# Performance work log

Hardware: AMD Instinct MI355X
Metric: run time of the kernel (lower is better)

Reference implementation:

```python
import jax, jax.numpy as jnp
import numpy as np

B, U, L, H, M = 4, 16, 128, 768, 256   # docs, utterances/doc, tokens/utt, hidden, mentions/doc
HID = 150                               # Score MLP hidden dim
N_CLUSTERS = 32


def setup_inputs() -> dict:
    key = jax.random.key(0)
    ks = jax.random.split(key, 8)
    hidden = jax.random.normal(ks[0], (B, U, L, H), jnp.float32)

    rng = np.random.default_rng(0)
    span_utt = rng.integers(0, U, (B, M))
    span_start = rng.integers(0, L - 8, (B, M))
    span_end = span_start + rng.integers(1, 9, (B, M))  # span length in [1, 8]

    # coreference labels: label[i, j] = 1 iff j is a true antecedent (j < i, same cluster);
    # if mention i has no antecedent, label[i, i] = 1 (the epsilon / new-entity slot).
    clusters = rng.integers(0, N_CLUSTERS, (B, M))
    same = clusters[:, :, None] == clusters[:, None, :]
    ant = same & np.tril(np.ones((M, M), bool), -1)
    labels = ant.astype(np.float32)
    diag = np.arange(M)
    labels[:, diag, diag] = (~ant.any(-1)).astype(np.float32)

    scale = 0.02
    W1 = jax.random.normal(ks[1], (3 * H, HID), jnp.float32) * scale
    W2 = jax.random.normal(ks[2], (HID, HID), jnp.float32) * scale
    W3 = jax.random.normal(ks[3], (HID, 1), jnp.float32) * scale
    return {
        "hidden": hidden,
        "span_utt": jnp.asarray(span_utt, jnp.int32),
        "span_start": jnp.asarray(span_start, jnp.int32),
        "span_end": jnp.asarray(span_end, jnp.int32),
        "labels": jnp.asarray(labels),
        "W1": W1, "b1": jnp.zeros((HID,), jnp.float32),
        "W2": W2, "b2": jnp.zeros((HID,), jnp.float32),
        "W3": W3, "b3": jnp.zeros((1,), jnp.float32),
    }


def reference(hidden, span_utt, span_start, span_end, labels, W1, b1, W2, b2, W3, b3):
    # ---- span mean-pooling (EntityEncoder, aggr='mean') ----
    pos = jnp.arange(L)
    mask = (pos[None, None, :] >= span_start[..., None]) & (pos[None, None, :] < span_end[..., None])
    w = mask.astype(hidden.dtype) / (span_end - span_start)[..., None].astype(hidden.dtype)  # [B,M,L]
    gathered = jnp.take_along_axis(hidden, span_utt[:, :, None, None], axis=1)  # [B,M,L,H]
    pooled = jnp.einsum('bml,bmlh->bmh', w, gathered)  # [B,M,H]

    # ---- pairwise antecedent scoring (PairScorer / Score MLP, dropout=eval) ----
    ii, jj = np.tril_indices(M, -1)  # static pair indices, P = M(M-1)/2
    # concat(i_g, j_g, i_g*j_g) @ W1  ==  i_g@W1a + j_g@W1b + (i_g*j_g)@W1c
    W1a, W1b, W1c = W1[:H], W1[H:2 * H], W1[2 * H:]
    hi = pooled @ W1a   # [B,M,HID]
    hj = pooled @ W1b   # [B,M,HID]
    prod = pooled[:, ii] * pooled[:, jj]                    # [B,P,H]
    h1 = jax.nn.relu(hi[:, ii] + hj[:, jj] + prod @ W1c + b1)
    h2 = jax.nn.relu(h1 @ W2 + b2)
    s = (h2 @ W3 + b3)[..., 0]  # [B,P]

    # ---- per-mention ragged softmax, padded to [M, M] with -1000 ----
    # row i has logits s_ij for j<i plus epsilon=0 at j=i (diagonal of zeros matrix)
    logits = jnp.zeros((B, M, M), hidden.dtype).at[:, ii, jj].set(s)
    valid = jnp.tril(jnp.ones((M, M), bool))
    probs = jax.nn.softmax(jnp.where(valid, logits, -1e30), axis=-1)
    probs = jnp.where(valid, probs, jnp.asarray(-1000.0, hidden.dtype))

    # ---- compute_loss ----
    eps = 1e-8
    prob_sum = jnp.sum(jnp.clip(probs * labels, eps, 1.0 - eps), axis=-1)  # [B,M]
    loss = -jnp.sum(jnp.log(prob_sum))
    return loss
```

## Files before the change

kernel.cpp:

```cpp
#include <hip/hip_runtime.h>
#include <hip/hip_bf16.h>

#define B_ 4
#define U_ 16
#define L_ 128
#define H_ 768
#define M_ 256
#define HID_ 150

typedef _Float16 half8 __attribute__((ext_vector_type(8)));
typedef _Float16 half4t __attribute__((ext_vector_type(4)));
typedef float floatx4 __attribute__((ext_vector_type(4)));
typedef float floatx16 __attribute__((ext_vector_type(16)));

__device__ __forceinline__ void gl_lds16(const _Float16* g, _Float16* l)
{
    __builtin_amdgcn_global_load_lds(
        (const __attribute__((address_space(1))) unsigned int*)g,
        (__attribute__((address_space(3))) unsigned int*)l, 16, 0, 0);
}

__global__ __launch_bounds__(256) void prep_pool_kernel(
    const float* __restrict__ W1, const float* __restrict__ W2,
    const float* __restrict__ b2, const float* __restrict__ W3,
    const float* __restrict__ hidden, const int* __restrict__ sutt,
    const int* __restrict__ sstart, const int* __restrict__ send,
    _Float16* __restrict__ W1cs, _Float16* __restrict__ W2s,
    _Float16* __restrict__ W1abs, float2* __restrict__ bw,
    _Float16* __restrict__ pooledh)
{
    if (blockIdx.x >= 1540) {
        const int bm = (blockIdx.x - 1540) * 4 + (threadIdx.x >> 6);
        const int lane = threadIdx.x & 63;
        const int b  = bm >> 8;
        const int u  = sutt[bm];
        const int st = sstart[bm];
        const int en = send[bm];
        const float inv = 1.0f / (float)(en - st);
        const float* src = hidden + ((size_t)(b * U_ + u) * L_) * H_ + lane * 12;
        float4 s[3];
        #pragma unroll
        for (int q = 0; q < 3; ++q) s[q] = make_float4(0.f, 0.f, 0.f, 0.f);
        for (int l = st; l < en; ++l) {
            const float* p = src + (size_t)l * H_;
            #pragma unroll
            for (int q = 0; q < 3; ++q) {
                float4 v = *(const float4*)(p + q * 4);
                s[q].x += v.x; s[q].y += v.y; s[q].z += v.z; s[q].w += v.w;
            }
        }
        _Float16* gp = pooledh + (size_t)bm * H_ + lane * 12;
        #pragma unroll
        for (int q = 0; q < 3; ++q) {
            half4t hv;
            hv[0] = (_Float16)(s[q].x * inv); hv[1] = (_Float16)(s[q].y * inv);
            hv[2] = (_Float16)(s[q].z * inv); hv[3] = (_Float16)(s[q].w * inv);
            *(half4t*)(gp + q * 4) = hv;
        }
        return;
    }
    int idx = blockIdx.x * 256 + threadIdx.x;
    if (blockIdx.x == 0 && threadIdx.x < 160) {
        int n = threadIdx.x;
        bw[n] = (n < HID_) ? make_float2(b2[n], W3[n]) : make_float2(0.f, 0.f);
    }
    if (idx < 122880) {
        int k = idx / 160, n = idx - k * 160;
        float v = (n < HID_) ? W1[(size_t)(2 * H_ + k) * HID_ + n] : 0.f;
        W1cs[(k >> 4) * 2560 + (n >> 5) * 512 +
             (((n & 31) | (((k >> 3) & 1) << 5)) << 3) + (k & 7)] = (_Float16)v;
        return;
    }
    idx -= 122880;
    if (idx < 25600) {
        int k = idx / 160, n = idx - k * 160;
        float v = (k < HID_ && n < HID_) ? W2[(size_t)k * HID_ + n] : 0.f;
        W2s[(k >> 4) * 2560 + (n >> 5) * 512 +
            (((n & 31) | (((k >> 3) & 1) << 5)) << 3) + (k & 7)] = (_Float16)v;
        return;
    }
    idx -= 25600;
    if (idx < 245760) {
        int k = idx / 320, n = idx - k * 320;
        float v = 0.f;
        if (n < HID_) v = W1[(size_t)k * HID_ + n];
        else if (n >= 160 && n < 160 + HID_) v = W1[(size_t)(H_ + k) * HID_ + (n - 160)];
        W1abs[(k >> 5) * 10240 + (n >> 4) * 512 +
              (((n & 15) | (((k >> 3) & 3) << 4)) << 3) + (k & 7)] = (_Float16)v;
    }
}

__global__ __launch_bounds__(256) void hihj_kernel(
    const _Float16* __restrict__ pooledh, const float* __restrict__ b1,
    const _Float16* __restrict__ W1abs,
    float* __restrict__ hiF, float* __restrict__ hjT)
{
    __shared__ __align__(16) _Float16 spool[16 * 776];
    const int blk = blockIdx.x;
    const int tid = threadIdx.x;
    for (int e = tid; e < 16 * 96; e += 256) {
        int r = e / 96, c = e - r * 96;
        *(half8*)&spool[r * 776 + c * 8] =
            *(const half8*)&pooledh[(size_t)(blk * 16 + r) * H_ + c * 8];
    }
    __syncthreads();

    const int w = tid >> 6, lane = tid & 63;
    const int g = lane >> 4, l15 = lane & 15;
    floatx4 acc[5];
    #pragma unroll
    for (int u5 = 0; u5 < 5; ++u5) acc[u5] = (floatx4){0.f, 0.f, 0.f, 0.f};
    const _Float16* aB = &spool[l15 * 776 + g * 8];
    for (int kc = 0; kc < 24; ++kc) {
        half8 av = *(const half8*)(aB + kc * 32);
        #pragma unroll
        for (int u5 = 0; u5 < 5; ++u5) {
            const int u = w * 5 + u5;
            half8 bv = *(const half8*)(W1abs + (size_t)((kc * 20 + u) * 64 + lane) * 8);
            acc[u5] = __builtin_amdgcn_mfma_f32_16x16x32_f16(av, bv, acc[u5], 0, 0, 0);
        }
    }
    const int row0 = blk * 16 + g * 4;
    #pragma unroll
    for (int u5 = 0; u5 < 5; ++u5) {
        const int n = (w * 5 + u5) * 16 + l15;
        if (n < HID_) {
            float b1v = b1[n];
            #pragma unroll
            for (int r = 0; r < 4; ++r)
                hiF[(size_t)(row0 + r) * 160 + n] = acc[u5][r] + b1v;
        } else if (n >= 160 && n < 160 + HID_) {
            *(float4*)&hjT[(size_t)(n - 160) * 1024 + row0] =
                make_float4(acc[u5][0], acc[u5][1], acc[u5][2], acc[u5][3]);
        }
    }
}

__global__ __launch_bounds__(128, 2) void pair_mlp_kernel(
    const _Float16* __restrict__ pooledh,
    const float* __restrict__ hiF, const float* __restrict__ hjT,
    const _Float16* __restrict__ W1cs, const _Float16* __restrict__ W2s,
    const float2* __restrict__ bw, const float* __restrict__ b3,
    float* __restrict__ logits)
{
    __shared__ __align__(16) _Float16 smem[3 * 5120];

    int q = blockIdx.x;
    const int b = q / 576;
    int r = q - b * 576;
    int jt = 0;
    while (r >= 128 - 16 * jt) { r -= 128 - 16 * jt; ++jt; }
    const int p = 16 * jt + r;
    const int i0 = 2 * p, j0 = jt * 32;
    const int bm = b * M_;
    const int w = threadIdx.x >> 6;
    const int lane = threadIdx.x & 63;
    const int c31 = lane & 31;
    const int hw = lane >> 5;

    _Float16* h1w = smem + w * 5440;

    const _Float16* pjp = pooledh + (size_t)(bm + j0 + c31) * H_ + (hw << 3);
    const _Float16* pip = pooledh + (size_t)(bm + i0 + w) * H_ + (hw << 3);

    floatx16 acc1[5];
    #pragma unroll
    for (int t1 = 0; t1 < 5; ++t1)
        #pragma unroll
        for (int e = 0; e < 16; ++e) acc1[t1][e] = 0.f;

    {
        const _Float16* gW = W1cs + (size_t)(5 * w) * 512 + lane * 8;
        #pragma unroll
        for (int c = 0; c < 5; ++c)
            gl_lds16(gW + c * 512, smem + (5 * w + c) * 512);
        #pragma unroll
        for (int c = 0; c < 5; ++c)
            gl_lds16(gW + 5120 + c * 512, smem + 5120 + (5 * w + c) * 512);
    }
    half8 Apj0[2], Apj1[2], Ai0[2], Ai1[2];
    Apj0[0] = *(const half8*)(pjp);
    Apj1[0] = *(const half8*)(pjp + 16);
    Ai0[0]  = *(const half8*)(pip);
    Ai1[0]  = *(const half8*)(pip + 16);
    asm volatile("s_waitcnt vmcnt(11)" ::: "memory");
    __builtin_amdgcn_s_barrier();
    __builtin_amdgcn_sched_barrier(0);

    #pragma unroll
    for (int kc = 0; kc < 24; ++kc) {
        const int cur = kc & 1, nxt = (kc + 1) & 1;
        const _Float16* Wcur = smem + (kc % 3) * 5120;
        if (kc < 23) {
            const int kb = (kc + 1) * 32;
            Apj0[nxt] = *(const half8*)(pjp + kb);
            Apj1[nxt] = *(const half8*)(pjp + kb + 16);
            Ai0[nxt]  = *(const half8*)(pip + kb);
            Ai1[nxt]  = *(const half8*)(pip + kb + 16);
        }
        if (kc < 22) {
            const _Float16* gW = W1cs + (size_t)(kc + 2) * 5120
                                 + (5 * w) * 512 + lane * 8;
            _Float16* Wd = smem + ((kc + 2) % 3) * 5120;
            #pragma unroll
            for (int c = 0; c < 5; ++c)
                gl_lds16(gW + c * 512, Wd + (5 * w + c) * 512);
        }
        {
            half8 a = Ai0[cur] * Apj0[cur];
            #pragma unroll
            for (int t1 = 0; t1 < 5; ++t1) {
                half8 wf = *(const half8*)&Wcur[t1 * 512 + lane * 8];
                acc1[t1] = __builtin_amdgcn_mfma_f32_32x32x16_f16(wf, a, acc1[t1], 0, 0, 0);
            }
        }
        {
            half8 a = Ai1[cur] * Apj1[cur];
            #pragma unroll
            for (int t1 = 0; t1 < 5; ++t1) {
                half8 wf = *(const half8*)&Wcur[(5 + t1) * 512 + lane * 8];
                acc1[t1] = __builtin_amdgcn_mfma_f32_32x32x16_f16(wf, a, acc1[t1], 0, 0, 0);
            }
        }
        if (kc < 22)       asm volatile("s_waitcnt vmcnt(11)" ::: "memory");
        else if (kc == 22) asm volatile("s_waitcnt vmcnt(6)" ::: "memory");
        if (kc < 23) {
            __builtin_amdgcn_s_barrier();
            __builtin_amdgcn_sched_barrier(0);
        }
    }
    __syncthreads();

    const int jcol = bm + j0 + c31;
    #pragma unroll
    for (int t1 = 0; t1 < 5; ++t1) {
        #pragma unroll
        for (int qd = 0; qd < 4; ++qd) {
            const int n1 = t1 * 32 + 8 * qd + 4 * hw;
            float hj0 = hjT[(size_t)(n1 + 0) * 1024 + jcol];
            float hj1 = hjT[(size_t)(n1 + 1) * 1024 + jcol];
            float hj2 = hjT[(size_t)(n1 + 2) * 1024 + jcol];
            float hj3 = hjT[(size_t)(n1 + 3) * 1024 + jcol];
            float4 hiv = *(const float4*)&hiF[(size_t)(bm + i0 + w) * 160 + n1];
            half4t hv;
            hv[0] = (_Float16)fmaxf(acc1[t1][4 * qd + 0] + hiv.x + hj0, 0.f);
            hv[1] = (_Float16)fmaxf(acc1[t1][4 * qd + 1] + hiv.y + hj1, 0.f);
            hv[2] = (_Float16)fmaxf(acc1[t1][4 * qd + 2] + hiv.z + hj2, 0.f);
            hv[3] = (_Float16)fmaxf(acc1[t1][4 * qd + 3] + hiv.w + hj3, 0.f);
            *(half4t*)&h1w[c31 * 170 + n1] = hv;
        }
    }
    __syncthreads();

    const float b3v = b3[0];
    floatx16 acc2[5];
    #pragma unroll
    for (int t2 = 0; t2 < 5; ++t2)
        #pragma unroll
        for (int e = 0; e < 16; ++e) acc2[t2][e] = 0.f;

    half8 W2b[2][5], h1b[2];
    #pragma unroll
    for (int c = 0; c < 2; ++c) {
        const _Float16* wb = W2s + (size_t)(c * 5) * 512 + lane * 8;
        #pragma unroll
        for (int t2 = 0; t2 < 5; ++t2) W2b[c][t2] = *(const half8*)(wb + t2 * 512);
        h1b[c] = *(const half8*)&h1w[c31 * 170 + c * 16 + hw * 8];
    }
    for (int kc2 = 0; kc2 < 10; ++kc2) {
        const int cur = kc2 & 1;
        half8 nw[5], nh;
        if (kc2 < 8) {
            const _Float16* wb = W2s + (size_t)((kc2 + 2) * 5) * 512 + lane * 8;
            #pragma unroll
            for (int t2 = 0; t2 < 5; ++t2) nw[t2] = *(const half8*)(wb + t2 * 512);
            nh = *(const half8*)&h1w[c31 * 170 + (kc2 + 2) * 16 + hw * 8];
        }
        #pragma unroll
        for (int t2 = 0; t2 < 5; ++t2)
            acc2[t2] = __builtin_amdgcn_mfma_f32_32x32x16_f16(
                W2b[cur][t2], h1b[cur], acc2[t2], 0, 0, 0);
        if (kc2 < 8) {
            #pragma unroll
            for (int t2 = 0; t2 < 5; ++t2) W2b[cur][t2] = nw[t2];
            h1b[cur] = nh;
        }
    }

    float sown = 0.f;
    #pragma unroll
    for (int t2 = 0; t2 < 5; ++t2) {
        #pragma unroll
        for (int qd = 0; qd < 4; ++qd) {
            const int n2 = t2 * 32 + 8 * qd + 4 * hw;
            float4 bw01 = *(const float4*)&bw[n2];
            float4 bw23 = *(const float4*)&bw[n2 + 2];
            sown += fmaxf(acc2[t2][4 * qd + 0] + bw01.x, 0.f) * bw01.y;
            sown += fmaxf(acc2[t2][4 * qd + 1] + bw01.z, 0.f) * bw01.w;
            sown += fmaxf(acc2[t2][4 * qd + 2] + bw23.x, 0.f) * bw23.y;
            sown += fmaxf(acc2[t2][4 * qd + 3] + bw23.z, 0.f) * bw23.w;
        }
    }
    float s = sown + __shfl_xor(sown, 32);
    const int i = i0 + w;
    const int j = j0 + c31;
    if (lane < 32 && j < i)
        logits[(size_t)(bm + i) * M_ + j] = s + b3v;
}

__global__ __launch_bounds__(256) void loss_kernel(
    const float* __restrict__ logits, const float* __restrict__ labels,
    float* __restrict__ out)
{
    const int bm = blockIdx.x;
    const int i  = bm & (M_ - 1);
    const int j  = threadIdx.x;
    __shared__ float red[4];
    __shared__ float bcast;

    float val = (j < i) ? logits[(size_t)bm * M_ + j]
                        : ((j == i) ? 0.0f : -1e30f);

    float m = val;
    #pragma unroll
    for (int off = 32; off >= 1; off >>= 1) m = fmaxf(m, __shfl_down(m, off, 64));
    const int wave = j >> 6, lane = j & 63;
    if (lane == 0) red[wave] = m;
    __syncthreads();
    if (j == 0) bcast = fmaxf(fmaxf(red[0], red[1]), fmaxf(red[2], red[3]));
    __syncthreads();
    const float mm = bcast;

    float e = (j <= i) ? expf(val - mm) : 0.0f;
    float s = e;
    #pragma unroll
    for (int off = 32; off >= 1; off >>= 1) s += __shfl_down(s, off, 64);
    __syncthreads();
    if (lane == 0) red[wave] = s;
    __syncthreads();
    if (j == 0) bcast = red[0] + red[1] + red[2] + red[3];
    __syncthreads();
    const float ssum = bcast;

    float prob = (j <= i) ? (e / ssum) : -1000.0f;
    float lab = labels[(size_t)bm * M_ + j];
    float tv = prob * lab;
    tv = fminf(fmaxf(tv, 1e-8f), 1.0f - 1e-8f);
    float rs = tv;
    #pragma unroll
    for (int off = 32; off >= 1; off >>= 1) rs += __shfl_down(rs, off, 64);
    __syncthreads();
    if (lane == 0) red[wave] = rs;
    __syncthreads();
    if (j == 0) atomicAdd(out, -logf(red[0] + red[1] + red[2] + red[3]));
}

extern "C" void kernel_launch(void* const* d_in, const int* in_sizes, int n_in,
                              void* d_out, int out_size, void* d_ws, size_t ws_size,
                              hipStream_t stream)
{
    const float* hidden = (const float*)d_in[0];
    const int*   sutt   = (const int*)d_in[1];
    const int*   sstart = (const int*)d_in[2];
    const int*   send   = (const int*)d_in[3];
    const float* labels = (const float*)d_in[4];
    const float* W1     = (const float*)d_in[5];
    const float* b1     = (const float*)d_in[6];
    const float* W2     = (const float*)d_in[7];
    const float* b2     = (const float*)d_in[8];
    const float* W3     = (const float*)d_in[9];
    const float* b3     = (const float*)d_in[10];

    float* ws = (float*)d_ws;
    float*    hiF     = ws;
    float*    hjT     = ws + 163840;
    float*    logits  = ws + 327680;
    float2*   bw      = (float2*)(ws + 589824);
    _Float16* pooledh = (_Float16*)(ws + 590144);
    _Float16* W1cs    = (_Float16*)(ws + 983360);
    _Float16* W2s     = (_Float16*)(ws + 1106240);
    _Float16* W1abs   = (_Float16*)(ws + 1119040);
    float* out = (float*)d_out;

    hipMemsetAsync(d_out, 0, sizeof(float), stream);

    prep_pool_kernel<<<dim3(1796), 256, 0, stream>>>(
        W1, W2, b2, W3, hidden, sutt, sstart, send,
        W1cs, W2s, W1abs, bw, pooledh);
    hihj_kernel<<<dim3(64), 256, 0, stream>>>(pooledh, b1, W1abs, hiF, hjT);
    pair_mlp_kernel<<<dim3(576 * B_), 128, 0, stream>>>(pooledh, hiF, hjT,
                                                        W1cs, W2s, bw, b3, logits);
    loss_kernel<<<dim3(B_ * M_), 256, 0, stream>>>(logits, labels, out);
}
```

Before: 196.2 us.

## Widen pair tile to 64 j-columns and use single-wave loss rows

The pair MLP block now covers 64 antecedent columns instead of 32. Each W1c fragment read from LDS feeds two MFMAs, and the i-row loads and W1c streaming are shared across twice the pairs. Grid size drops from 576 to 320 blocks per document. The cost is doubled layer-1 accumulator registers, which may hurt occupancy or cause spills, and a serialized second-layer pass per 32-column half. Separately, the loss kernel handles each row with one 64-thread wave using four elements per lane and xor shuffles, removing the LDS reductions and barriers.

```diff
diff --git a/kernel.cpp b/kernel.cpp
--- a/kernel.cpp
+++ b/kernel.cpp
@@ -146,12 +146,14 @@
     __shared__ __align__(16) _Float16 smem[3 * 5120];
 
     int q = blockIdx.x;
-    const int b = q / 576;
-    int r = q - b * 576;
-    int jt = 0;
-    while (r >= 128 - 16 * jt) { r -= 128 - 16 * jt; ++jt; }
-    const int p = 16 * jt + r;
-    const int i0 = 2 * p, j0 = jt * 32;
+    const int b = q / 320;
+    int r = q - b * 320;
+    int jt64, p;
+    if (r < 128)      { jt64 = 0; p = r; }
+    else if (r < 224) { jt64 = 1; p = 32 + (r - 128); }
+    else if (r < 288) { jt64 = 2; p = 64 + (r - 224); }
+    else              { jt64 = 3; p = 96 + (r - 288); }
+    const int i0 = 2 * p, j0 = jt64 * 64;
     const int bm = b * M_;
     const int w = threadIdx.x >> 6;
     const int lane = threadIdx.x & 63;
@@ -160,14 +162,17 @@
 
     _Float16* h1w = smem + w * 5440;
 
-    const _Float16* pjp = pooledh + (size_t)(bm + j0 + c31) * H_ + (hw << 3);
+    const _Float16* pj0 = pooledh + (size_t)(bm + j0 + c31) * H_ + (hw << 3);
+    const _Float16* pj1 = pooledh + (size_t)(bm + j0 + 32 + c31) * H_ + (hw << 3);
     const _Float16* pip = pooledh + (size_t)(bm + i0 + w) * H_ + (hw << 3);
 
-    floatx16 acc1[5];
-    #pragma unroll
-    for (int t1 = 0; t1 < 5; ++t1)
-        #pragma unroll
-        for (int e = 0; e < 16; ++e) acc1[t1][e] = 0.f;
+    floatx16 acc1[2][5];
+    #pragma unroll
+    for (int f = 0; f < 2; ++f)
+        #pragma unroll
+        for (int t1 = 0; t1 < 5; ++t1)
+            #pragma unroll
+            for (int e = 0; e < 16; ++e) acc1[f][t1][e] = 0.f;
 
     {
         const _Float16* gW = W1cs + (size_t)(5 * w) * 512 + lane * 8;
@@ -178,9 +183,11 @@
         for (int c = 0; c < 5; ++c)
             gl_lds16(gW + 5120 + c * 512, smem + 5120 + (5 * w + c) * 512);
     }
-    half8 Apj0[2], Apj1[2], Ai0[2], Ai1[2];
-    Apj0[0] = *(const half8*)(pjp);
-    Apj1[0] = *(const half8*)(pjp + 16);
+    half8 Aj00[2], Aj01[2], Aj10[2], Aj11[2], Ai0[2], Ai1[2];
+    Aj00[0] = *(const half8*)(pj0);
+    Aj01[0] = *(const half8*)(pj0 + 16);
+    Aj10[0] = *(const half8*)(pj1);
+    Aj11[0] = *(const half8*)(pj1 + 16);
     Ai0[0]  = *(const half8*)(pip);
     Ai1[0]  = *(const half8*)(pip + 16);
     asm volatile("s_waitcnt vmcnt(11)" ::: "memory");
@@ -193,8 +200,10 @@
         const _Float16* Wcur = smem + (kc % 3) * 5120;
         if (kc < 23) {
             const int kb = (kc + 1) * 32;
-            Apj0[nxt] = *(const half8*)(pjp + kb);
-            Apj1[nxt] = *(const half8*)(pjp + kb + 16);
+            Aj00[nxt] = *(const half8*)(pj0 + kb);
+            Aj01[nxt] = *(const half8*)(pj0 + kb + 16);
+            Aj10[nxt] = *(const half8*)(pj1 + kb);
+            Aj11[nxt] = *(const half8*)(pj1 + kb + 16);
             Ai0[nxt]  = *(const half8*)(pip + kb);
             Ai1[nxt]  = *(const half8*)(pip + kb + 16);
         }
@@ -207,19 +216,23 @@
                 gl_lds16(gW + c * 512, Wd + (5 * w + c) * 512);
         }
         {
-            half8 a = Ai0[cur] * Apj0[cur];
+            half8 a0 = Ai0[cur] * Aj00[cur];
+            half8 a1 = Ai0[cur] * Aj10[cur];
             #pragma unroll
             for (int t1 = 0; t1 < 5; ++t1) {
                 half8 wf = *(const half8*)&Wcur[t1 * 512 + lane * 8];
-                acc1[t1] = __builtin_amdgcn_mfma_f32_32x32x16_f16(wf, a, acc1[t1], 0, 0, 0);
+                acc1[0][t1] = __builtin_amdgcn_mfma_f32_32x32x16_f16(wf, a0, acc1[0][t1], 0, 0, 0);
+                acc1[1][t1] = __builtin_amdgcn_mfma_f32_32x32x16_f16(wf, a1, acc1[1][t1], 0, 0, 0);
             }
         }
         {
-            half8 a = Ai1[cur] * Apj1[cur];
+            half8 a0 = Ai1[cur] * Aj01[cur];
+            half8 a1 = Ai1[cur] * Aj11[cur];
             #pragma unroll
             for (int t1 = 0; t1 < 5; ++t1) {
                 half8 wf = *(const half8*)&Wcur[(5 + t1) * 512 + lane * 8];
-                acc1[t1] = __builtin_amdgcn_mfma_f32_32x32x16_f16(wf, a, acc1[t1], 0, 0, 0);
+                acc1[0][t1] = __builtin_amdgcn_mfma_f32_32x32x16_f16(wf, a0, acc1[0][t1], 0, 0, 0);
+                acc1[1][t1] = __builtin_amdgcn_mfma_f32_32x32x16_f16(wf, a1, acc1[1][t1], 0, 0, 0);
             }
         }
         if (kc < 22)       asm volatile("s_waitcnt vmcnt(11)" ::: "memory");
@@ -231,128 +244,130 @@
     }
     __syncthreads();
 
-    const int jcol = bm + j0 + c31;
-    #pragma unroll
-    for (int t1 = 0; t1 < 5; ++t1) {
-        #pragma unroll
-        for (int qd = 0; qd < 4; ++qd) {
-            const int n1 = t1 * 32 + 8 * qd + 4 * hw;
-            float hj0 = hjT[(size_t)(n1 + 0) * 1024 + jcol];
-            float hj1 = hjT[(size_t)(n1 + 1) * 1024 + jcol];
-            float hj2 = hjT[(size_t)(n1 + 2) * 1024 + jcol];
-            float hj3 = hjT[(size_t)(n1 + 3) * 1024 + jcol];
-            float4 hiv = *(const float4*)&hiF[(size_t)(bm + i0 + w) * 160 + n1];
-            half4t hv;
-            hv[0] = (_Float16)fmaxf(acc1[t1][4 * qd + 0] + hiv.x + hj0, 0.f);
-            hv[1] = (_Float16)fmaxf(acc1[t1][4 * qd + 1] + hiv.y + hj1, 0.f);
-            hv[2] = (_Float16)fmaxf(acc1[t1][4 * qd + 2] + hiv.z + hj2, 0.f);
-            hv[3] = (_Float16)fmaxf(acc1[t1][4 * qd + 3] + hiv.w + hj3, 0.f);
-            *(half4t*)&h1w[c31 * 170 + n1] = hv;
-        }
-    }
-    __syncthreads();
-
     const float b3v = b3[0];
-    floatx16 acc2[5];
-    #pragma unroll
-    for (int t2 = 0; t2 < 5; ++t2)
-        #pragma unroll
-        for (int e = 0; e < 16; ++e) acc2[t2][e] = 0.f;
-
-    half8 W2b[2][5], h1b[2];
-    #pragma unroll
-    for (int c = 0; c < 2; ++c) {
-        const _Float16* wb = W2s + (size_t)(c * 5) * 512 + lane * 8;
-        #pragma unroll
-        for (int t2 = 0; t2 < 5; ++t2) W2b[c][t2] = *(const half8*)(wb + t2 * 512);
-        h1b[c] = *(const half8*)&h1w[c31 * 170 + c * 16 + hw * 8];
-    }
-    for (int kc2 = 0; kc2 < 10; ++kc2) {
-        const int cur = kc2 & 1;
-        half8 nw[5], nh;
-        if (kc2 < 8) {
-            const _Float16* wb = W2s + (size_t)((kc2 + 2) * 5) * 512 + lane * 8;
-            #pragma unroll
-            for (int t2 = 0; t2 < 5; ++t2) nw[t2] = *(const half8*)(wb + t2 * 512);
-            nh = *(const half8*)&h1w[c31 * 170 + (kc2 + 2) * 16 + hw * 8];
-        }
+    const int irow = i0 + w;
+    #pragma unroll
+    for (int f = 0; f < 2; ++f) {
+        __syncthreads();
+        const int jcol = bm + j0 + f * 32 + c31;
+        #pragma unroll
+        for (int t1 = 0; t1 < 5; ++t1) {
+            #pragma unroll
+            for (int qd = 0; qd < 4; ++qd) {
+                const int n1 = t1 * 32 + 8 * qd + 4 * hw;
+                float hj0 = hjT[(size_t)(n1 + 0) * 1024 + jcol];
+                float hj1 = hjT[(size_t)(n1 + 1) * 1024 + jcol];
+                float hj2 = hjT[(size_t)(n1 + 2) * 1024 + jcol];
+                float hj3 = hjT[(size_t)(n1 + 3) * 1024 + jcol];
+                float4 hiv = *(const float4*)&hiF[(size_t)(bm + irow) * 160 + n1];
+                half4t hv;
+                hv[0] = (_Float16)fmaxf(acc1[f][t1][4 * qd + 0] + hiv.x + hj0, 0.f);
+                hv[1] = (_Float16)fmaxf(acc1[f][t1][4 * qd + 1] + hiv.y + hj1, 0.f);
+                hv[2] = (_Float16)fmaxf(acc1[f][t1][4 * qd + 2] + hiv.z + hj2, 0.f);
+                hv[3] = (_Float16)fmaxf(acc1[f][t1][4 * qd + 3] + hiv.w + hj3, 0.f);
+                *(half4t*)&h1w[c31 * 170 + n1] = hv;
+            }
+        }
+        __syncthreads();
+
+        floatx16 acc2[5];
         #pragma unroll
         for (int t2 = 0; t2 < 5; ++t2)
-            acc2[t2] = __builtin_amdgcn_mfma_f32_32x32x16_f16(
-                W2b[cur][t2], h1b[cur], acc2[t2], 0, 0, 0);
-        if (kc2 < 8) {
-            #pragma unroll
-            for (int t2 = 0; t2 < 5; ++t2) W2b[cur][t2] = nw[t2];
-            h1b[cur] = nh;
-        }
-    }
-
-    float sown = 0.f;
-    #pragma unroll
-    for (int t2 = 0; t2 < 5; ++t2) {
-        #pragma unroll
-        for (int qd = 0; qd < 4; ++qd) {
-            const int n2 = t2 * 32 + 8 * qd + 4 * hw;
-            float4 bw01 = *(const float4*)&bw[n2];
-            float4 bw23 = *(const float4*)&bw[n2 + 2];
-            sown += fmaxf(acc2[t2][4 * qd + 0] + bw01.x, 0.f) * bw01.y;
-            sown += fmaxf(acc2[t2][4 * qd + 1] + bw01.z, 0.f) * bw01.w;
-            sown += fmaxf(acc2[t2][4 * qd + 2] + bw23.x, 0.f) * bw23.y;
-            sown += fmaxf(acc2[t2][4 * qd + 3] + bw23.z, 0.f) * bw23.w;
-        }
-    }
-    float s = sown + __shfl_xor(sown, 32);
-    const int i = i0 + w;
-    const int j = j0 + c31;
-    if (lane < 32 && j < i)
-        logits[(size_t)(bm + i) * M_ + j] = s + b3v;
-}
-
-__global__ __launch_bounds__(256) void loss_kernel(
+            #pragma unroll
+            for (int e = 0; e < 16; ++e) acc2[t2][e] = 0.f;
+
+        half8 W2b[2][5], h1b[2];
+        #pragma unroll
+        for (int c = 0; c < 2; ++c) {
+            const _Float16* wb = W2s + (size_t)(c * 5) * 512 + lane * 8;
+            #pragma unroll
+            for (int t2 = 0; t2 < 5; ++t2) W2b[c][t2] = *(const half8*)(wb + t2 * 512);
+            h1b[c] = *(const half8*)&h1w[c31 * 170 + c * 16 + hw * 8];
+        }
+        for (int kc2 = 0; kc2 < 10; ++kc2) {
+            const int cur = kc2 & 1;
+            half8 nw[5], nh;
+            if (kc2 < 8) {
+                const _Float16* wb = W2s + (size_t)((kc2 + 2) * 5) * 512 + lane * 8;
+                #pragma unroll
+                for (int t2 = 0; t2 < 5; ++t2) nw[t2] = *(const half8*)(wb + t2 * 512);
+                nh = *(const half8*)&h1w[c31 * 170 + (kc2 + 2) * 16 + hw * 8];
+            }
+            #pragma unroll
+            for (int t2 = 0; t2 < 5; ++t2)
+                acc2[t2] = __builtin_amdgcn_mfma_f32_32x32x16_f16(
+                    W2b[cur][t2], h1b[cur], acc2[t2], 0, 0, 0);
+            if (kc2 < 8) {
+                #pragma unroll
+                for (int t2 = 0; t2 < 5; ++t2) W2b[cur][t2] = nw[t2];
+                h1b[cur] = nh;
+            }
+        }
+
+        float sown = 0.f;
+        #pragma unroll
+        for (int t2 = 0; t2 < 5; ++t2) {
+            #pragma unroll
+            for (int qd = 0; qd < 4; ++qd) {
+                const int n2 = t2 * 32 + 8 * qd + 4 * hw;
+                float4 bw01 = *(const float4*)&bw[n2];
+                float4 bw23 = *(const float4*)&bw[n2 + 2];
+                sown += fmaxf(acc2[t2][4 * qd + 0] + bw01.x, 0.f) * bw01.y;
+                sown += fmaxf(acc2[t2][4 * qd + 1] + bw01.z, 0.f) * bw01.w;
+                sown += fmaxf(acc2[t2][4 * qd + 2] + bw23.x, 0.f) * bw23.y;
+                sown += fmaxf(acc2[t2][4 * qd + 3] + bw23.z, 0.f) * bw23.w;
+            }
+        }
+        float s = sown + __shfl_xor(sown, 32);
+        const int j = j0 + f * 32 + c31;
+        if (lane < 32 && j < irow)
+            logits[(size_t)(bm + irow) * M_ + j] = s + b3v;
+    }
+}
+
+__global__ __launch_bounds__(64) void loss_kernel(
     const float* __restrict__ logits, const float* __restrict__ labels,
     float* __restrict__ out)
 {
     const int bm = blockIdx.x;
     const int i  = bm & (M_ - 1);
-    const int j  = threadIdx.x;
-    __shared__ float red[4];
-    __shared__ float bcast;
-
-    float val = (j < i) ? logits[(size_t)bm * M_ + j]
-                        : ((j == i) ? 0.0f : -1e30f);
-
-    float m = val;
-    #pragma unroll
-    for (int off = 32; off >= 1; off >>= 1) m = fmaxf(m, __shfl_down(m, off, 64));
-    const int wave = j >> 6, lane = j & 63;
-    if (lane == 0) red[wave] = m;
-    __syncthreads();
-    if (j == 0) bcast = fmaxf(fmaxf(red[0], red[1]), fmaxf(red[2], red[3]));
-    __syncthreads();
-    const float mm = bcast;
-
-    float e = (j <= i) ? expf(val - mm) : 0.0f;
-    float s = e;
-    #pragma unroll
-    for (int off = 32; off >= 1; off >>= 1) s += __shfl_down(s, off, 64);
-    __syncthreads();
-    if (lane == 0) red[wave] = s;
-    __syncthreads();
-    if (j == 0) bcast = red[0] + red[1] + red[2] + red[3];
-    __syncthreads();
-    const float ssum = bcast;
-
-    float prob = (j <= i) ? (e / ssum) : -1000.0f;
-    float lab = labels[(size_t)bm * M_ + j];
-    float tv = prob * lab;
-    tv = fminf(fmaxf(tv, 1e-8f), 1.0f - 1e-8f);
-    float rs = tv;
-    #pragma unroll
-    for (int off = 32; off >= 1; off >>= 1) rs += __shfl_down(rs, off, 64);
-    __syncthreads();
-    if (lane == 0) red[wave] = rs;
-    __syncthreads();
-    if (j == 0) atomicAdd(out, -logf(red[0] + red[1] + red[2] + red[3]));
+    const int lane = threadIdx.x;
+
+    float val[4];
+    #pragma unroll
+    for (int qq = 0; qq < 4; ++qq) {
+        const int j = qq * 64 + lane;
+        val[qq] = (j < i) ? logits[(size_t)bm * M_ + j]
+                          : ((j == i) ? 0.0f : -1e30f);
+    }
+    float m = fmaxf(fmaxf(val[0], val[1]), fmaxf(val[2], val[3]));
+    #pragma unroll
+    for (int off = 32; off >= 1; off >>= 1) m = fmaxf(m, __shfl_xor(m, off));
+
+    float s = 0.f;
+    float e[4];
+    #pragma unroll
+    for (int qq = 0; qq < 4; ++qq) {
+        const int j = qq * 64 + lane;
+        e[qq] = (j <= i) ? expf(val[qq] - m) : 0.0f;
+        s += e[qq];
+    }
+    #pragma unroll
+    for (int off = 32; off >= 1; off >>= 1) s += __shfl_xor(s, off);
+    const float inv_s = 1.0f / s;
+
+    float rs = 0.f;
+    #pragma unroll
+    for (int qq = 0; qq < 4; ++qq) {
+        const int j = qq * 64 + lane;
+        float prob = (j <= i) ? (e[qq] * inv_s) : -1000.0f;
+        float tv = prob * labels[(size_t)bm * M_ + j];
+        rs += fminf(fmaxf(tv, 1e-8f), 1.0f - 1e-8f);
+    }
+    #pragma unroll
+    for (int off = 32; off >= 1; off >>= 1) rs += __shfl_xor(rs, off);
+
+    if (lane == 0) atomicAdd(out, -logf(rs));
 }
 
 extern "C" void kernel_launch(void* const* d_in, const int* in_sizes, int n_in,
@@ -388,7 +403,7 @@
         W1, W2, b2, W3, hidden, sutt, sstart, send,
         W1cs, W2s, W1abs, bw, pooledh);
     hihj_kernel<<<dim3(64), 256, 0, stream>>>(pooledh, b1, W1abs, hiF, hjT);
-    pair_mlp_kernel<<<dim3(576 * B_), 128, 0, stream>>>(pooledh, hiF, hjT,
+    pair_mlp_kernel<<<dim3(320 * B_), 128, 0, stream>>>(pooledh, hiF, hjT,
                                                         W1cs, W2s, bw, b3, logits);
-    loss_kernel<<<dim3(B_ * M_), 256, 0, stream>>>(logits, labels, out);
-}
+    loss_kernel<<<dim3(B_ * M_), 64, 0, stream>>>(logits, labels, out);
+}
```

Result: slower. 293.8 us (+49.8%).
